# Optimization experiments

Hardware: AMD Instinct MI355X
Metric: run time of the kernel (lower is better)

Reference implementation:

```python
import jax, jax.numpy as jnp
import numpy as np

B, D, H = 64, 768, 512            # batch, bert hidden, classifier hidden_dim
G0, C0 = 8192, 8                  # level-0 meta labels, children per meta
G1, C1 = 65536, 11                # level-1 meta labels, children per meta (incl. pad)
L = 670091                        # num labels; pad id == L, table has L+1 rows
K1, K2 = 32, 64                   # candidates_topk


def setup_inputs() -> dict:
    key = jax.random.key(0)
    ks = jax.random.split(key, 14)
    rn = lambda k, shp, s=1.0: jax.random.normal(k, shp, jnp.float32) * s
    w = 0.02  # xavier-ish init scale
    inp = {
        'feat5':   rn(ks[0], (B, D)),
        'feat8':   rn(ks[1], (B, D)),
        'featcat': rn(ks[2], (B, 3 * D)),
        'W0': rn(ks[3], (D, H), w),     'b0': jnp.zeros((H,), jnp.float32),
        'W1': rn(ks[4], (D, H), w),     'b1': jnp.zeros((H,), jnp.float32),
        'W2': rn(ks[5], (3 * D, H), w), 'b2': jnp.zeros((H,), jnp.float32),
        'E0': rn(ks[6], (G0, H), w),
        'E1': rn(ks[7], (G1, H), w),
        # padding row (index L) is zero, per self.Cn[-1].weight[-1].data.fill_(0)
        'E2': rn(ks[8], (L + 1, H), w).at[-1].set(0.0),
        'g0': jax.random.randint(ks[9], (G0, C0), 0, G1, dtype=jnp.int32),
        'g1': jax.random.randint(ks[10], (G1, C1), 0, L + 1, dtype=jnp.int32),
    }
    return inp


def reference(feat5, feat8, featcat, W0, b0, W1, b1, W2, b2, E0, E1, E2, g0, g1):
    gelu = lambda x: jax.nn.gelu(x, approximate=False)  # torch nn.GELU default (erf)
    # Cn_hidden (dropout is identity at eval)
    h0 = gelu(feat5 @ W0 + b0)      # [B,H]
    h1 = gelu(feat8 @ W1 + b1)      # [B,H]
    h2 = gelu(featcat @ W2 + b2)    # [B,H]

    # ---- level 0: score all G0 meta-labels (dense bmm) ----
    logits0 = jnp.einsum('gh,bh->bg', E0, h0)            # [B,G0]
    p0 = jax.nn.sigmoid(logits0)
    prev0 = jax.lax.stop_gradient(p0)                    # prev_logits = scores.detach()

    # ---- level 1: topk routing + gather + bmm ----
    sc1, idx1 = jax.lax.top_k(prev0, K1)                 # [B,K1]; prev_cands is arange -> identity map
    cands1 = g0[idx1].reshape(B, K1 * C0)                # [B,K1*C0] level-1 meta ids
    gsc1 = jnp.repeat(sc1, C0, axis=1)                   # candidates_scores flattened
    logits1 = jnp.einsum('bch,bh->bc', E1[cands1], h1)   # [B,K1*C0]
    p1 = jax.nn.sigmoid(logits1)
    w1 = p1 * gsc1
    prev1 = jax.lax.stop_gradient(p1)

    # ---- level 2 (final): topk routing into padded label groups ----
    sc2, idx2 = jax.lax.top_k(prev1, K2)                 # [B,K2]
    meta2 = jnp.take_along_axis(cands1, idx2, axis=1)    # indices into g1
    cands2 = g1[meta2].reshape(B, K2 * C1)               # [B,K2*C1] label ids (L == pad)
    gsc2 = jnp.repeat(sc2, C1, axis=1)
    logits2 = jnp.einsum('bch,bh->bc', E2[cands2], h2)   # pad rows of E2 are 0 -> logit 0
    # torch: where(logits==0, -inf, logits).sigmoid() -> pad positions score 0
    p2 = jnp.where(logits2 == 0.0, jnp.float32(0.0), jax.nn.sigmoid(logits2))
    w2 = p2 * gsc2

    return (p0, p1, p2, w1, w2, cands1, cands2)
```

## Files before the change

kernel.cpp:

```cpp
#include <hip/hip_runtime.h>
#include <math.h>

#define BB 64
#define D0 768
#define D2 2304
#define HH 512
#define BBHH (BB*HH)
#define NG0 8192
#define NC0 8
#define NCH1 11
#define TK1 32
#define TK2 64
#define NC1 (TK1*NC0)
#define NC2 (TK2*NCH1)
#define SPA 2
#define SPB 2
#define SPC 6
#define NSL (SPA+SPB+SPC)

__device__ __forceinline__ float sigmoidf_(float x){ return 1.0f/(1.0f+expf(-x)); }
__device__ __forceinline__ float geluf_(float x){ return 0.5f*x*(1.0f+erff(x*0.70710678118654752f)); }
__device__ __forceinline__ unsigned long long maxu64_(unsigned long long a, unsigned long long b){ return a>b?a:b; }

__device__ __forceinline__ unsigned long long bitonic256_desc(
    unsigned long long key, int tid, unsigned long long* sbuf)
{
  #pragma unroll
  for (int k = 2; k <= 256; k <<= 1) {
    #pragma unroll
    for (int j = k >> 1; j > 0; j >>= 1) {
      unsigned long long other;
      if (j >= 64) {
        __syncthreads();
        sbuf[tid] = key;
        __syncthreads();
        other = sbuf[tid ^ j];
      } else {
        other = __shfl_xor(key, j, 64);
      }
      bool keep_max = ((tid & j) == 0) == ((tid & k) == 0);
      key = keep_max ? (key > other ? key : other)
                     : (key < other ? key : other);
    }
  }
  return key;
}

__global__ __launch_bounds__(256) void gemm_h_kernel(
    const float* __restrict__ feat5, const float* __restrict__ feat8,
    const float* __restrict__ featcat,
    const float* __restrict__ W0, const float* __restrict__ W1,
    const float* __restrict__ W2, float* __restrict__ P)
{
  __shared__ __align__(16) float At[32][68];
  __shared__ __align__(16) float Bt[32][36];
  const int bid = blockIdx.x, tid = threadIdx.x;
  const float* X; const float* W; int Dm, split, jt, slice;
  if (bid < 32)      { X=feat5;   W=W0; Dm=D0; int l=bid;    split=l&1; jt=(l>>1)*32; slice=split; }
  else if (bid < 64) { X=feat8;   W=W1; Dm=D0; int l=bid-32; split=l&1; jt=(l>>1)*32; slice=SPA+split; }
  else               { X=featcat; W=W2; Dm=D2; int l=bid-64; split=l%6; jt=(l/6)*32;  slice=SPA+SPB+split; }
  float* Pb = P + (size_t)slice*BBHH;
  int k0 = split*384;
  int ti = tid >> 4, tj = tid & 15;
  float acc[4][2] = {};
  for (int ks = 0; ks < 384; ks += 32) {
    #pragma unroll
    for (int it = 0; it < 2; ++it) {
      int q = tid + it*256;
      int b = q & 63, kq = q >> 6;
      float4 v = *(const float4*)(X + (size_t)b*Dm + k0 + ks + kq*4);
      At[kq*4+0][b]=v.x; At[kq*4+1][b]=v.y; At[kq*4+2][b]=v.z; At[kq*4+3][b]=v.w;
    }
    {
      int j4 = tid & 7, kk = tid >> 3;
      float4 v = *(const float4*)(W + (size_t)(k0+ks+kk)*HH + jt + j4*4);
      *(float4*)&Bt[kk][j4*4] = v;
    }
    __syncthreads();
    #pragma unroll
    for (int k = 0; k < 32; ++k) {
      float4 a = *(const float4*)&At[k][ti*4];
      float2 b = *(const float2*)&Bt[k][tj*2];
      float av[4] = {a.x,a.y,a.z,a.w};
      float bv[2] = {b.x,b.y};
      #pragma unroll
      for (int r=0;r<4;++r)
        #pragma unroll
        for (int c=0;c<2;++c) acc[r][c] += av[r]*bv[c];
    }
    __syncthreads();
  }
  #pragma unroll
  for (int r=0;r<4;++r)
    #pragma unroll
    for (int c=0;c<2;++c)
      Pb[(size_t)(ti*4+r)*HH + jt + tj*2 + c] = acc[r][c];
}

__global__ __launch_bounds__(256,2) void level0_kernel(
    const float* __restrict__ P, const float* __restrict__ b0v,
    const float* __restrict__ E0, float* __restrict__ p0out)
{
  __shared__ __align__(16) float At[32][20];
  __shared__ __align__(16) float Bt[32][68];
  const int bid = blockIdx.x, tid = threadIdx.x;
  const int btile = bid & 3;
  const int gt = bid >> 2;
  const int ti = tid >> 4, tj = tid & 15;
  float acc[4] = {};
  for (int ks = 0; ks < HH; ks += 32) {
    {
      int bb = tid & 15, kq = tid >> 4;
      float2 a = make_float2(0.f, 0.f);
      #pragma unroll
      for (int s=0;s<SPA;++s){
        float2 p = *(const float2*)(P + (size_t)s*BBHH
                        + (size_t)(btile*16+bb)*HH + ks + kq*2);
        a.x += p.x; a.y += p.y;
      }
      float2 bv = *(const float2*)(b0v + ks + kq*2);
      At[kq*2+0][bb] = geluf_(a.x + bv.x);
      At[kq*2+1][bb] = geluf_(a.y + bv.y);
    }
    #pragma unroll
    for (int it=0; it<2; ++it) {
      int q = tid + it*256; int g = q & 63, kq = q >> 6;
      float4 v = *(const float4*)(E0 + (size_t)(gt*64+g)*HH + ks + kq*4);
      Bt[kq*4+0][g]=v.x; Bt[kq*4+1][g]=v.y; Bt[kq*4+2][g]=v.z; Bt[kq*4+3][g]=v.w;
    }
    __syncthreads();
    #pragma unroll
    for (int k=0;k<32;++k) {
      float a = At[k][ti];
      float4 b = *(const float4*)&Bt[k][tj*4];
      acc[0] += a*b.x; acc[1] += a*b.y; acc[2] += a*b.z; acc[3] += a*b.w;
    }
    __syncthreads();
  }
  #pragma unroll
  for (int c=0;c<4;++c)
    p0out[(size_t)(btile*16 + ti)*NG0 + gt*64 + tj*4 + c] = sigmoidf_(acc[c]);
}

__global__ __launch_bounds__(256) void topk1_level1_kernel(
    const float* __restrict__ p0, const int* __restrict__ g0,
    const float* __restrict__ P, const float* __restrict__ b1v,
    const float* __restrict__ E1,
    int* __restrict__ cands1_i, float* __restrict__ o_c1,
    float* __restrict__ o_p1, float* __restrict__ o_w1)
{
  const int bid = blockIdx.x, tid = threadIdx.x;
  const int b = bid & 63, q = bid >> 6;
  const int lane = tid & 63, wid = tid >> 6;
  __shared__ float h1row[HH];
  __shared__ unsigned long long sbuf[256];
  __shared__ unsigned long long slist[256];
  __shared__ float s_sc[TK1];
  __shared__ int   s_idx[TK1];
  __shared__ int   scnt;
  {
    int j = tid*2;
    float ax=0.f, ay=0.f;
    #pragma unroll
    for (int s=0;s<SPB;++s){
      float2 v = *(const float2*)(P + (size_t)(SPA+s)*BBHH + (size_t)b*HH + j);
      ax += v.x; ay += v.y;
    }
    float2 bv = *(const float2*)(b1v + j);
    h1row[j]   = geluf_(ax + bv.x);
    h1row[j+1] = geluf_(ay + bv.y);
  }
  if (tid==0) scnt = 0;
  const float* row = p0 + (size_t)b*NG0;
  const float4* rp = (const float4*)(row + tid*32);
  unsigned long long m = 0ull;
  #pragma unroll
  for (int t=0;t<8;++t){
    float4 v = rp[t];
    unsigned i0 = (unsigned)(tid*32 + t*4);
    m = maxu64_(m, ((unsigned long long)__float_as_uint(v.x)<<32) | (unsigned long long)(0xFFFFFFFFu-(i0+0)));
    m = maxu64_(m, ((unsigned long long)__float_as_uint(v.y)<<32) | (unsigned long long)(0xFFFFFFFFu-(i0+1)));
    m = maxu64_(m, ((unsigned long long)__float_as_uint(v.z)<<32) | (unsigned long long)(0xFFFFFFFFu-(i0+2)));
    m = maxu64_(m, ((unsigned long long)__float_as_uint(v.w)<<32) | (unsigned long long)(0xFFFFFFFFu-(i0+3)));
  }
  __syncthreads();
  unsigned long long sk = bitonic256_desc(m, tid, sbuf);
  __syncthreads();
  sbuf[tid] = sk;
  __syncthreads();
  unsigned long long t32 = sbuf[31];
  __syncthreads();
  #pragma unroll
  for (int t=0;t<8;++t){
    float4 v = rp[t];
    unsigned i0 = (unsigned)(tid*32 + t*4);
    unsigned long long k0 = ((unsigned long long)__float_as_uint(v.x)<<32) | (unsigned long long)(0xFFFFFFFFu-(i0+0));
    unsigned long long k1 = ((unsigned long long)__float_as_uint(v.y)<<32) | (unsigned long long)(0xFFFFFFFFu-(i0+1));
    unsigned long long k2 = ((unsigned long long)__float_as_uint(v.z)<<32) | (unsigned long long)(0xFFFFFFFFu-(i0+2));
    unsigned long long k3 = ((unsigned long long)__float_as_uint(v.w)<<32) | (unsigned long long)(0xFFFFFFFFu-(i0+3));
    if (k0 >= t32) { int p = atomicAdd(&scnt,1); if (p<256) slist[p]=k0; }
    if (k1 >= t32) { int p = atomicAdd(&scnt,1); if (p<256) slist[p]=k1; }
    if (k2 >= t32) { int p = atomicAdd(&scnt,1); if (p<256) slist[p]=k2; }
    if (k3 >= t32) { int p = atomicAdd(&scnt,1); if (p<256) slist[p]=k3; }
  }
  __syncthreads();
  int cnt = scnt;
  unsigned long long key2 = (tid < cnt) ? slist[tid] : 0ull;
  key2 = bitonic256_desc(key2, tid, sbuf);
  __syncthreads();
  sbuf[tid] = key2;
  __syncthreads();
  if (tid < TK1) {
    unsigned long long w = sbuf[tid];
    s_idx[tid] = (int)(0xFFFFFFFFu - (unsigned)(w & 0xFFFFFFFFull));
    s_sc[tid]  = __uint_as_float((unsigned)(w>>32));
  }
  __syncthreads();
  if (q==0 && tid < NC1) {
    int k = tid >> 3, c = tid & 7;
    int cand = g0[(size_t)s_idx[k]*NC0 + c];
    cands1_i[(size_t)b*NC1+tid] = cand;
    o_c1[(size_t)b*NC1+tid] = (float)cand;
  }
  float4 ha = *(const float4*)&h1row[lane*8];
  float4 hb = *(const float4*)&h1row[lane*8+4];
  #pragma unroll
  for (int j=0;j<4;++j){
    int cbase = (q + 4*j)*16 + wid*4;
    int id0 = g0[(size_t)s_idx[(cbase+0)>>3]*NC0 + ((cbase+0)&7)];
    int id1 = g0[(size_t)s_idx[(cbase+1)>>3]*NC0 + ((cbase+1)&7)];
    int id2 = g0[(size_t)s_idx[(cbase+2)>>3]*NC0 + ((cbase+2)&7)];
    int id3 = g0[(size_t)s_idx[(cbase+3)>>3]*NC0 + ((cbase+3)&7)];
    const float4* pe0 = (const float4*)(E1 + (size_t)id0*HH);
    const float4* pe1 = (const float4*)(E1 + (size_t)id1*HH);
    const float4* pe2 = (const float4*)(E1 + (size_t)id2*HH);
    const float4* pe3 = (const float4*)(E1 + (size_t)id3*HH);
    float4 a0=pe0[lane*2], c0=pe0[lane*2+1];
    float4 a1=pe1[lane*2], c1=pe1[lane*2+1];
    float4 a2=pe2[lane*2], c2=pe2[lane*2+1];
    float4 a3=pe3[lane*2], c3=pe3[lane*2+1];
    float s0 = ha.x*a0.x+ha.y*a0.y+ha.z*a0.z+ha.w*a0.w + hb.x*c0.x+hb.y*c0.y+hb.z*c0.z+hb.w*c0.w;
    float s1 = ha.x*a1.x+ha.y*a1.y+ha.z*a1.z+ha.w*a1.w + hb.x*c1.x+hb.y*c1.y+hb.z*c1.z+hb.w*c1.w;
    float s2 = ha.x*a2.x+ha.y*a2.y+ha.z*a2.z+ha.w*a2.w + hb.x*c2.x+hb.y*c2.y+hb.z*c2.z+hb.w*c2.w;
    float s3 = ha.x*a3.x+ha.y*a3.y+ha.z*a3.z+ha.w*a3.w + hb.x*c3.x+hb.y*c3.y+hb.z*c3.z+hb.w*c3.w;
    #pragma unroll
    for (int off=1; off<64; off<<=1) {
      s0 += __shfl_xor(s0, off);
      s1 += __shfl_xor(s1, off);
      s2 += __shfl_xor(s2, off);
      s3 += __shfl_xor(s3, off);
    }
    if (lane==0) {
      float p;
      p = sigmoidf_(s0); o_p1[(size_t)b*NC1+cbase+0]=p; o_w1[(size_t)b*NC1+cbase+0]=p*s_sc[(cbase+0)>>3];
      p = sigmoidf_(s1); o_p1[(size_t)b*NC1+cbase+1]=p; o_w1[(size_t)b*NC1+cbase+1]=p*s_sc[(cbase+1)>>3];
      p = sigmoidf_(s2); o_p1[(size_t)b*NC1+cbase+2]=p; o_w1[(size_t)b*NC1+cbase+2]=p*s_sc[(cbase+2)>>3];
      p = sigmoidf_(s3); o_p1[(size_t)b*NC1+cbase+3]=p; o_w1[(size_t)b*NC1+cbase+3]=p*s_sc[(cbase+3)>>3];
    }
  }
}

__global__ __launch_bounds__(256,2) void topk2_level2_kernel(
    const float* __restrict__ p1, const int* __restrict__ cands1_i,
    const int* __restrict__ g1,
    const float* __restrict__ P, const float* __restrict__ b2v,
    const float* __restrict__ E2,
    float* __restrict__ o_c2, float* __restrict__ o_p2, float* __restrict__ o_w2)
{
  const int bid = blockIdx.x, tid = threadIdx.x;
  const int b = bid & 63, q = bid >> 6;
  const int lane = tid & 63, wid = tid >> 6;
  __shared__ float h2row[HH];
  __shared__ unsigned long long sbuf[256];
  __shared__ float s_sc[TK2];
  __shared__ int   s_idx[TK2];
  __shared__ int   c1row[NC1];
  {
    int j = tid*2;
    float ax=0.f, ay=0.f;
    #pragma unroll
    for (int s=0;s<SPC;++s){
      float2 v = *(const float2*)(P + (size_t)(SPA+SPB+s)*BBHH + (size_t)b*HH + j);
      ax += v.x; ay += v.y;
    }
    float2 bv = *(const float2*)(b2v + j);
    h2row[j]   = geluf_(ax + bv.x);
    h2row[j+1] = geluf_(ay + bv.y);
  }
  c1row[tid] = cands1_i[(size_t)b*NC1 + tid];
  float v = p1[(size_t)b*NC1 + tid];
  unsigned long long key = ((unsigned long long)__float_as_uint(v)<<32) |
                           (unsigned long long)(0xFFFFFFFFu - (unsigned)tid);
  __syncthreads();
  key = bitonic256_desc(key, tid, sbuf);
  __syncthreads();
  sbuf[tid] = key;
  __syncthreads();
  if (tid < TK2) {
    unsigned long long w = sbuf[tid];
    s_idx[tid] = (int)(0xFFFFFFFFu - (unsigned)(w & 0xFFFFFFFFull));
    s_sc[tid]  = __uint_as_float((unsigned)(w>>32));
  }
  __syncthreads();
  if (q==0) {
    for (int e=tid; e<NC2; e+=256) {
      int k = e/NCH1, c = e - k*NCH1;
      int meta = c1row[s_idx[k]];
      int cand = g1[(size_t)meta*NCH1 + c];
      o_c2[(size_t)b*NC2+e] = (float)cand;
    }
  }
  float4 ha = *(const float4*)&h2row[lane*8];
  float4 hb = *(const float4*)&h2row[lane*8+4];
  for (int j=0;j<11;++j){
    int cbase = q*88 + j*8 + wid*2;
    int k0i = (cbase+0)/NCH1, c0i = (cbase+0) - k0i*NCH1;
    int k1i = (cbase+1)/NCH1, c1i = (cbase+1) - k1i*NCH1;
    int id0 = g1[(size_t)c1row[s_idx[k0i]]*NCH1 + c0i];
    int id1 = g1[(size_t)c1row[s_idx[k1i]]*NCH1 + c1i];
    const float4* pe0 = (const float4*)(E2 + (size_t)id0*HH);
    const float4* pe1 = (const float4*)(E2 + (size_t)id1*HH);
    float4 a0=pe0[lane*2], c0=pe0[lane*2+1];
    float4 a1=pe1[lane*2], c1=pe1[lane*2+1];
    float s0 = ha.x*a0.x+ha.y*a0.y+ha.z*a0.z+ha.w*a0.w + hb.x*c0.x+hb.y*c0.y+hb.z*c0.z+hb.w*c0.w;
    float s1 = ha.x*a1.x+ha.y*a1.y+ha.z*a1.z+ha.w*a1.w + hb.x*c1.x+hb.y*c1.y+hb.z*c1.z+hb.w*c1.w;
    #pragma unroll
    for (int off=1; off<64; off<<=1) {
      s0 += __shfl_xor(s0, off);
      s1 += __shfl_xor(s1, off);
    }
    if (lane==0) {
      float p;
      p = (s0==0.0f)?0.0f:sigmoidf_(s0); o_p2[(size_t)b*NC2+cbase+0]=p; o_w2[(size_t)b*NC2+cbase+0]=p*s_sc[k0i];
      p = (s1==0.0f)?0.0f:sigmoidf_(s1); o_p2[(size_t)b*NC2+cbase+1]=p; o_w2[(size_t)b*NC2+cbase+1]=p*s_sc[k1i];
    }
  }
}

extern "C" void kernel_launch(void* const* d_in, const int* in_sizes, int n_in,
                              void* d_out, int out_size, void* d_ws, size_t ws_size,
                              hipStream_t stream) {
  const float* feat5   = (const float*)d_in[0];
  const float* feat8   = (const float*)d_in[1];
  const float* featcat = (const float*)d_in[2];
  const float* W0 = (const float*)d_in[3];
  const float* b0 = (const float*)d_in[4];
  const float* W1 = (const float*)d_in[5];
  const float* b1 = (const float*)d_in[6];
  const float* W2 = (const float*)d_in[7];
  const float* b2 = (const float*)d_in[8];
  const float* E0 = (const float*)d_in[9];
  const float* E1 = (const float*)d_in[10];
  const float* E2 = (const float*)d_in[11];
  const int*   g0 = (const int*)d_in[12];
  const int*   g1 = (const int*)d_in[13];

  float* out = (float*)d_out;
  float* ws  = (float*)d_ws;

  size_t off = 0;
  float* P = ws + off; off += (size_t)NSL*BBHH;
  int*   cands1_i = (int*)(ws + off); off += (size_t)BB*NC1;

  float* o_p0 = out;
  float* o_p1 = o_p0 + (size_t)BB*NG0;
  float* o_p2 = o_p1 + (size_t)BB*NC1;
  float* o_w1 = o_p2 + (size_t)BB*NC2;
  float* o_w2 = o_w1 + (size_t)BB*NC1;
  float* o_c1 = o_w2 + (size_t)BB*NC2;
  float* o_c2 = o_c1 + (size_t)BB*NC1;

  gemm_h_kernel<<<dim3(160), dim3(256), 0, stream>>>(feat5, feat8, featcat, W0, W1, W2, P);
  level0_kernel<<<dim3(512), dim3(256), 0, stream>>>(P, b0, E0, o_p0);
  topk1_level1_kernel<<<dim3(256), dim3(256), 0, stream>>>(o_p0, g0, P, b1, E1,
      cands1_i, o_c1, o_p1, o_w1);
  topk2_level2_kernel<<<dim3(512), dim3(256), 0, stream>>>(o_p1, cands1_i, g1, P, b2, E2,
      o_c2, o_p2, o_w2);
}
```

Measured before the change: 90.05 us.

## Prefetch gathered embedding rows one iteration ahead and remap level-0 block order

In the level-1 and level-2 gather kernels, all candidate ids are now resolved up front, and each iteration loads the next iteration's embedding rows before reducing the current ones. This software pipelining is meant to hide the latency of dependent random gathers from E1 and E2. Separately, the level-0 kernel changes how block ids map to (g-tile, b-tile), which changes which blocks run together and how they share E0 tiles in cache. The cost is higher register pressure from the extra prefetch buffers and the id arrays, which could lower occupancy.

```diff
diff --git a/kernel.cpp b/kernel.cpp
--- a/kernel.cpp
+++ b/kernel.cpp
@@ -21,6 +21,9 @@
 __device__ __forceinline__ float sigmoidf_(float x){ return 1.0f/(1.0f+expf(-x)); }
 __device__ __forceinline__ float geluf_(float x){ return 0.5f*x*(1.0f+erff(x*0.70710678118654752f)); }
 __device__ __forceinline__ unsigned long long maxu64_(unsigned long long a, unsigned long long b){ return a>b?a:b; }
+__device__ __forceinline__ float dot8_(float4 ha, float4 hb, float4 a, float4 c){
+  return ha.x*a.x+ha.y*a.y+ha.z*a.z+ha.w*a.w + hb.x*c.x+hb.y*c.y+hb.z*c.z+hb.w*c.w;
+}
 
 __device__ __forceinline__ unsigned long long bitonic256_desc(
     unsigned long long key, int tid, unsigned long long* sbuf)
@@ -104,8 +107,9 @@
   __shared__ __align__(16) float At[32][20];
   __shared__ __align__(16) float Bt[32][68];
   const int bid = blockIdx.x, tid = threadIdx.x;
-  const int btile = bid & 3;
-  const int gt = bid >> 2;
+  const int slot = bid >> 3;
+  const int gt = (bid & 7) * 16 + (slot >> 2);
+  const int btile = slot & 3;
   const int ti = tid >> 4, tj = tid & 15;
   float acc[4] = {};
   for (int ks = 0; ks < HH; ks += 32) {
@@ -224,25 +228,37 @@
   }
   float4 ha = *(const float4*)&h1row[lane*8];
   float4 hb = *(const float4*)&h1row[lane*8+4];
+  int cid[4][4];
   #pragma unroll
   for (int j=0;j<4;++j){
     int cbase = (q + 4*j)*16 + wid*4;
-    int id0 = g0[(size_t)s_idx[(cbase+0)>>3]*NC0 + ((cbase+0)&7)];
-    int id1 = g0[(size_t)s_idx[(cbase+1)>>3]*NC0 + ((cbase+1)&7)];
-    int id2 = g0[(size_t)s_idx[(cbase+2)>>3]*NC0 + ((cbase+2)&7)];
-    int id3 = g0[(size_t)s_idx[(cbase+3)>>3]*NC0 + ((cbase+3)&7)];
-    const float4* pe0 = (const float4*)(E1 + (size_t)id0*HH);
-    const float4* pe1 = (const float4*)(E1 + (size_t)id1*HH);
-    const float4* pe2 = (const float4*)(E1 + (size_t)id2*HH);
-    const float4* pe3 = (const float4*)(E1 + (size_t)id3*HH);
-    float4 a0=pe0[lane*2], c0=pe0[lane*2+1];
-    float4 a1=pe1[lane*2], c1=pe1[lane*2+1];
-    float4 a2=pe2[lane*2], c2=pe2[lane*2+1];
-    float4 a3=pe3[lane*2], c3=pe3[lane*2+1];
-    float s0 = ha.x*a0.x+ha.y*a0.y+ha.z*a0.z+ha.w*a0.w + hb.x*c0.x+hb.y*c0.y+hb.z*c0.z+hb.w*c0.w;
-    float s1 = ha.x*a1.x+ha.y*a1.y+ha.z*a1.z+ha.w*a1.w + hb.x*c1.x+hb.y*c1.y+hb.z*c1.z+hb.w*c1.w;
-    float s2 = ha.x*a2.x+ha.y*a2.y+ha.z*a2.z+ha.w*a2.w + hb.x*c2.x+hb.y*c2.y+hb.z*c2.z+hb.w*c2.w;
-    float s3 = ha.x*a3.x+ha.y*a3.y+ha.z*a3.z+ha.w*a3.w + hb.x*c3.x+hb.y*c3.y+hb.z*c3.z+hb.w*c3.w;
+    #pragma unroll
+    for (int u=0;u<4;++u)
+      cid[j][u] = g0[(size_t)s_idx[(cbase+u)>>3]*NC0 + ((cbase+u)&7)];
+  }
+  float4 a0,c0,a1,c1,a2,c2,a3,c3;
+  {
+    const float4* p0e=(const float4*)(E1+(size_t)cid[0][0]*HH);
+    const float4* p1e=(const float4*)(E1+(size_t)cid[0][1]*HH);
+    const float4* p2e=(const float4*)(E1+(size_t)cid[0][2]*HH);
+    const float4* p3e=(const float4*)(E1+(size_t)cid[0][3]*HH);
+    a0=p0e[lane*2]; c0=p0e[lane*2+1]; a1=p1e[lane*2]; c1=p1e[lane*2+1];
+    a2=p2e[lane*2]; c2=p2e[lane*2+1]; a3=p3e[lane*2]; c3=p3e[lane*2+1];
+  }
+  #pragma unroll
+  for (int j=0;j<4;++j){
+    float4 na0,nc0,na1,nc1,na2,nc2,na3,nc3;
+    if (j<3){
+      const float4* p0e=(const float4*)(E1+(size_t)cid[j+1][0]*HH);
+      const float4* p1e=(const float4*)(E1+(size_t)cid[j+1][1]*HH);
+      const float4* p2e=(const float4*)(E1+(size_t)cid[j+1][2]*HH);
+      const float4* p3e=(const float4*)(E1+(size_t)cid[j+1][3]*HH);
+      na0=p0e[lane*2]; nc0=p0e[lane*2+1]; na1=p1e[lane*2]; nc1=p1e[lane*2+1];
+      na2=p2e[lane*2]; nc2=p2e[lane*2+1]; na3=p3e[lane*2]; nc3=p3e[lane*2+1];
+    }
+    int cbase = (q + 4*j)*16 + wid*4;
+    float s0=dot8_(ha,hb,a0,c0), s1=dot8_(ha,hb,a1,c1);
+    float s2=dot8_(ha,hb,a2,c2), s3=dot8_(ha,hb,a3,c3);
     #pragma unroll
     for (int off=1; off<64; off<<=1) {
       s0 += __shfl_xor(s0, off);
@@ -257,6 +273,7 @@
       p = sigmoidf_(s2); o_p1[(size_t)b*NC1+cbase+2]=p; o_w1[(size_t)b*NC1+cbase+2]=p*s_sc[(cbase+2)>>3];
       p = sigmoidf_(s3); o_p1[(size_t)b*NC1+cbase+3]=p; o_w1[(size_t)b*NC1+cbase+3]=p*s_sc[(cbase+3)>>3];
     }
+    if (j<3){ a0=na0;c0=nc0;a1=na1;c1=nc1;a2=na2;c2=nc2;a3=na3;c3=nc3; }
   }
 }
 
@@ -312,18 +329,34 @@
   }
   float4 ha = *(const float4*)&h2row[lane*8];
   float4 hb = *(const float4*)&h2row[lane*8+4];
+  int cid0[11], cid1[11];
+  #pragma unroll
   for (int j=0;j<11;++j){
+    int cb = q*88 + j*8 + wid*2;
+    int k0i = (cb+0)/NCH1, c0i = (cb+0) - k0i*NCH1;
+    int k1i = (cb+1)/NCH1, c1i = (cb+1) - k1i*NCH1;
+    cid0[j] = g1[(size_t)c1row[s_idx[k0i]]*NCH1 + c0i];
+    cid1[j] = g1[(size_t)c1row[s_idx[k1i]]*NCH1 + c1i];
+  }
+  float4 a0,c0,a1,c1;
+  {
+    const float4* p0e=(const float4*)(E2+(size_t)cid0[0]*HH);
+    const float4* p1e=(const float4*)(E2+(size_t)cid1[0]*HH);
+    a0=p0e[lane*2]; c0=p0e[lane*2+1]; a1=p1e[lane*2]; c1=p1e[lane*2+1];
+  }
+  #pragma unroll
+  for (int j=0;j<11;++j){
+    float4 na0,nc0,na1,nc1;
+    if (j<10){
+      const float4* p0e=(const float4*)(E2+(size_t)cid0[j+1]*HH);
+      const float4* p1e=(const float4*)(E2+(size_t)cid1[j+1]*HH);
+      na0=p0e[lane*2]; nc0=p0e[lane*2+1]; na1=p1e[lane*2]; nc1=p1e[lane*2+1];
+    }
     int cbase = q*88 + j*8 + wid*2;
-    int k0i = (cbase+0)/NCH1, c0i = (cbase+0) - k0i*NCH1;
-    int k1i = (cbase+1)/NCH1, c1i = (cbase+1) - k1i*NCH1;
-    int id0 = g1[(size_t)c1row[s_idx[k0i]]*NCH1 + c0i];
-    int id1 = g1[(size_t)c1row[s_idx[k1i]]*NCH1 + c1i];
-    const float4* pe0 = (const float4*)(E2 + (size_t)id0*HH);
-    const float4* pe1 = (const float4*)(E2 + (size_t)id1*HH);
-    float4 a0=pe0[lane*2], c0=pe0[lane*2+1];
-    float4 a1=pe1[lane*2], c1=pe1[lane*2+1];
-    float s0 = ha.x*a0.x+ha.y*a0.y+ha.z*a0.z+ha.w*a0.w + hb.x*c0.x+hb.y*c0.y+hb.z*c0.z+hb.w*c0.w;
-    float s1 = ha.x*a1.x+ha.y*a1.y+ha.z*a1.z+ha.w*a1.w + hb.x*c1.x+hb.y*c1.y+hb.z*c1.z+hb.w*c1.w;
+    int k0i = (cbase+0)/NCH1;
+    int k1i = (cbase+1)/NCH1;
+    float s0 = dot8_(ha,hb,a0,c0);
+    float s1 = dot8_(ha,hb,a1,c1);
     #pragma unroll
     for (int off=1; off<64; off<<=1) {
       s0 += __shfl_xor(s0, off);
@@ -334,6 +367,7 @@
       p = (s0==0.0f)?0.0f:sigmoidf_(s0); o_p2[(size_t)b*NC2+cbase+0]=p; o_w2[(size_t)b*NC2+cbase+0]=p*s_sc[k0i];
       p = (s1==0.0f)?0.0f:sigmoidf_(s1); o_p2[(size_t)b*NC2+cbase+1]=p; o_w2[(size_t)b*NC2+cbase+1]=p*s_sc[k1i];
     }
+    if (j<10){ a0=na0;c0=nc0;a1=na1;c1=nc1; }
   }
 }
 
```

Result: no change. 88.51 us (-1.7%).
